# Kernel tuning notes

Hardware: AMD Instinct MI355X
Metric: run time of the kernel (lower is better)

## Reference

```python
import jax, jax.numpy as jnp
import numpy as np

B, N = 8192, 2048
_EPS = 1e-5


def setup_inputs() -> dict:
    key = jax.random.key(0)
    k1, k2, k3 = jax.random.split(key, 3)
    src = jax.random.normal(k1, (B, 3, N), dtype=jnp.float32)
    src_corr = jax.random.normal(k2, (B, 3, N), dtype=jnp.float32)
    weights = jax.random.uniform(k3, (B, N), dtype=jnp.float32)
    return {"src": src, "src_corr": src_corr, "weights": weights}


def reference(src, src_corr, weights):
    # src, src_corr: (B, 3, N); weights: (B, N)
    a = jnp.swapaxes(src, -1, -2)        # (B, N, 3)
    b = jnp.swapaxes(src_corr, -1, -2)   # (B, N, 3)
    w = weights[..., None]               # (B, N, 1)
    wn = w / (jnp.sum(w, axis=1, keepdims=True) + _EPS)
    centroid_a = jnp.sum(a * wn, axis=1)  # (B, 3)
    centroid_b = jnp.sum(b * wn, axis=1)  # (B, 3)
    a_c = a - centroid_a[:, None, :]
    b_c = b - centroid_b[:, None, :]
    # cov = a_c^T @ (b_c * wn) -> (B, 3, 3)
    cov = jnp.einsum('bnd,bne->bde', a_c, b_c * wn)
    u, s, vh = jnp.linalg.svd(cov, full_matrices=False)
    v = jnp.swapaxes(vh, -1, -2)
    ut = jnp.swapaxes(u, -1, -2)
    rot_pos = v @ ut
    v_neg = v.at[:, :, 2].multiply(-1.0)  # flip last column of v
    rot_neg = v_neg @ ut
    rot = jnp.where(jnp.linalg.det(rot_pos)[:, None, None] > 0, rot_pos, rot_neg)
    translation = centroid_b - jnp.einsum('bij,bj->bi', rot, centroid_a)  # (B, 3)
    return rot, translation
```

## Files before the change

kernel.cpp:

```cpp
#include <hip/hip_runtime.h>
#include <math.h>


constexpr int kB = 8192;
constexpr int kN = 2048;
constexpr float kEps = 1e-5f;
constexpr int kWavesPerBatch = 4;
constexpr int kIters = kN / 4 / 64 / kWavesPerBatch;

__global__ __launch_bounds__(256) void wproc_reduce(
    const float* __restrict__ src,
    const float* __restrict__ src_corr,
    const float* __restrict__ weights,
    float* __restrict__ ws)
{
    const int lane = threadIdx.x & 63;
    const int wave = threadIdx.x >> 6;
    const int b = blockIdx.x;

    const float* arow = src + (size_t)b * 3 * kN;
    const float* brow = src_corr + (size_t)b * 3 * kN;
    const float4* w4  = reinterpret_cast<const float4*>(weights + (size_t)b * kN);
    const float4* ax4 = reinterpret_cast<const float4*>(arow);
    const float4* ay4 = reinterpret_cast<const float4*>(arow + kN);
    const float4* az4 = reinterpret_cast<const float4*>(arow + 2 * kN);
    const float4* bx4 = reinterpret_cast<const float4*>(brow);
    const float4* by4 = reinterpret_cast<const float4*>(brow + kN);
    const float4* bz4 = reinterpret_cast<const float4*>(brow + 2 * kN);

    float acc[16];
#pragma unroll
    for (int i = 0; i < 16; ++i) acc[i] = 0.f;

#pragma unroll
    for (int it = 0; it < kIters; ++it) {
        const int idx = (wave * kIters + it) * 64 + lane;
        const float4 w  = w4[idx];
        const float4 ax = ax4[idx];
        const float4 ay = ay4[idx];
        const float4 az = az4[idx];
        const float4 bx = bx4[idx];
        const float4 by = by4[idx];
        const float4 bz = bz4[idx];
        const float wc[4]  = {w.x,  w.y,  w.z,  w.w};
        const float axc[4] = {ax.x, ax.y, ax.z, ax.w};
        const float ayc[4] = {ay.x, ay.y, ay.z, ay.w};
        const float azc[4] = {az.x, az.y, az.z, az.w};
        const float bxc[4] = {bx.x, bx.y, bx.z, bx.w};
        const float byc[4] = {by.x, by.y, by.z, by.w};
        const float bzc[4] = {bz.x, bz.y, bz.z, bz.w};
#pragma unroll
        for (int c = 0; c < 4; ++c) {
            const float ww  = wc[c];
            const float wax = ww * axc[c], way = ww * ayc[c], waz = ww * azc[c];
            const float bxx = bxc[c], byy = byc[c], bzz = bzc[c];
            acc[0]  += ww;
            acc[1]  += wax;                acc[2]  += way;                acc[3]  += waz;
            acc[4]  = fmaf(ww,  bxx, acc[4]);  acc[5]  = fmaf(ww,  byy, acc[5]);  acc[6]  = fmaf(ww,  bzz, acc[6]);
            acc[7]  = fmaf(wax, bxx, acc[7]);  acc[8]  = fmaf(wax, byy, acc[8]);  acc[9]  = fmaf(wax, bzz, acc[9]);
            acc[10] = fmaf(way, bxx, acc[10]); acc[11] = fmaf(way, byy, acc[11]); acc[12] = fmaf(way, bzz, acc[12]);
            acc[13] = fmaf(waz, bxx, acc[13]); acc[14] = fmaf(waz, byy, acc[14]); acc[15] = fmaf(waz, bzz, acc[15]);
        }
    }

#pragma unroll
    for (int i = 0; i < 16; ++i) {
        float v = acc[i];
#pragma unroll
        for (int off = 32; off > 0; off >>= 1)
            v += __shfl_down(v, off, 64);
        acc[i] = v;
    }

    __shared__ float part[kWavesPerBatch][16];
    if (lane == 0) {
#pragma unroll
        for (int i = 0; i < 16; ++i) part[wave][i] = acc[i];
    }
    __syncthreads();
    if (threadIdx.x < 16) {
        const int t = threadIdx.x;
        float s = part[0][t] + part[1][t] + part[2][t] + part[3][t];
        ws[(size_t)b * 16 + t] = s;
    }
}

__global__ __launch_bounds__(256) void wproc_solve(
    const float* __restrict__ ws,
    float* __restrict__ out)
{
    const int b = blockIdx.x * blockDim.x + threadIdx.x;
    if (b >= kB) return;

    float t[16];
#pragma unroll
    for (int i = 0; i < 4; ++i) {
        const float4 v = reinterpret_cast<const float4*>(ws + (size_t)b * 16)[i];
        t[4 * i] = v.x; t[4 * i + 1] = v.y; t[4 * i + 2] = v.z; t[4 * i + 3] = v.w;
    }

    const float W   = t[0];
    const float inv = 1.f / (W + kEps);
    const float S   = W * inv;
    float ca[3], cb[3];
#pragma unroll
    for (int d = 0; d < 3; ++d) { ca[d] = t[1 + d] * inv; cb[d] = t[4 + d] * inv; }

    float M[3][3];
    const float f2 = 2.f - S;
#pragma unroll
    for (int d = 0; d < 3; ++d)
#pragma unroll
        for (int e = 0; e < 3; ++e)
            M[d][e] = t[7 + 3 * d + e] * inv - ca[d] * cb[e] * f2;

    const float T  = M[0][0] + M[1][1] + M[2][2];
    const float cx = M[1][2] - M[2][1];
    const float cy = M[2][0] - M[0][2];
    const float cz = M[0][1] - M[1][0];
    float Nm[4][4];
    Nm[0][0] = T;
    Nm[0][1] = Nm[1][0] = cx;
    Nm[0][2] = Nm[2][0] = cy;
    Nm[0][3] = Nm[3][0] = cz;
    Nm[1][1] = 2.f * M[0][0] - T;
    Nm[2][2] = 2.f * M[1][1] - T;
    Nm[3][3] = 2.f * M[2][2] - T;
    Nm[1][2] = Nm[2][1] = M[0][1] + M[1][0];
    Nm[1][3] = Nm[3][1] = M[0][2] + M[2][0];
    Nm[2][3] = Nm[3][2] = M[1][2] + M[2][1];

    float Vv[4][4] = {{1,0,0,0},{0,1,0,0},{0,0,1,0},{0,0,0,1}};
    const int pp[6] = {0,0,0,1,1,2};
    const int qq[6] = {1,2,3,2,3,3};
    for (int sweep = 0; sweep < 6; ++sweep) {
        for (int r = 0; r < 6; ++r) {
            const int p = pp[r], q = qq[r];
            const float apq = Nm[p][q];
            if (fabsf(apq) < 1e-12f) continue;
            const float tau = (Nm[q][q] - Nm[p][p]) / (2.f * apq);
            const float tt  = copysignf(1.f, tau) / (fabsf(tau) + sqrtf(1.f + tau * tau));
            const float c   = 1.f / sqrtf(1.f + tt * tt);
            const float s   = tt * c;
            const float app = Nm[p][p], aqq = Nm[q][q];
            Nm[p][p] = app - tt * apq;
            Nm[q][q] = aqq + tt * apq;
            Nm[p][q] = Nm[q][p] = 0.f;
#pragma unroll
            for (int k = 0; k < 4; ++k) {
                if (k == p || k == q) continue;
                const float akp = Nm[k][p], akq = Nm[k][q];
                Nm[k][p] = Nm[p][k] = c * akp - s * akq;
                Nm[k][q] = Nm[q][k] = s * akp + c * akq;
            }
#pragma unroll
            for (int k = 0; k < 4; ++k) {
                const float vkp = Vv[k][p], vkq = Vv[k][q];
                Vv[k][p] = c * vkp - s * vkq;
                Vv[k][q] = s * vkp + c * vkq;
            }
        }
    }

    int jm = 0;
#pragma unroll
    for (int j = 1; j < 4; ++j) if (Nm[j][j] > Nm[jm][jm]) jm = j;
    float qw = Vv[0][jm], qx = Vv[1][jm], qy = Vv[2][jm], qz = Vv[3][jm];
    const float nq = 1.f / sqrtf(qw * qw + qx * qx + qy * qy + qz * qz);
    qw *= nq; qx *= nq; qy *= nq; qz *= nq;

    float R[3][3];
    R[0][0] = 1.f - 2.f * (qy * qy + qz * qz);
    R[0][1] = 2.f * (qx * qy - qw * qz);
    R[0][2] = 2.f * (qx * qz + qw * qy);
    R[1][0] = 2.f * (qx * qy + qw * qz);
    R[1][1] = 1.f - 2.f * (qx * qx + qz * qz);
    R[1][2] = 2.f * (qy * qz - qw * qx);
    R[2][0] = 2.f * (qx * qz - qw * qy);
    R[2][1] = 2.f * (qy * qz + qw * qx);
    R[2][2] = 1.f - 2.f * (qx * qx + qy * qy);

    float* ro = out + (size_t)b * 9;
#pragma unroll
    for (int i = 0; i < 3; ++i)
#pragma unroll
        for (int j = 0; j < 3; ++j)
            ro[3 * i + j] = R[i][j];

    float* to = out + (size_t)kB * 9 + (size_t)b * 3;
#pragma unroll
    for (int i = 0; i < 3; ++i)
        to[i] = cb[i] - (R[i][0] * ca[0] + R[i][1] * ca[1] + R[i][2] * ca[2]);
}

extern "C" void kernel_launch(void* const* d_in, const int* in_sizes, int n_in,
                              void* d_out, int out_size, void* d_ws, size_t ws_size,
                              hipStream_t stream) {
    const float* src      = (const float*)d_in[0];
    const float* src_corr = (const float*)d_in[1];
    const float* weights  = (const float*)d_in[2];
    float* out = (float*)d_out;
    float* ws  = (float*)d_ws;
    wproc_reduce<<<kB, 64 * kWavesPerBatch, 0, stream>>>(src, src_corr, weights, ws);
    wproc_solve<<<(kB + 255) / 256, 256, 0, stream>>>(ws, out);
}
```

Baseline: 443.2 us.

## Batch loads before compute, unroll Jacobi rotations statically, shrink solve blocks

In the reduce kernel, all global float4 loads are issued up front into register arrays before any accumulation, so more memory requests are in flight per wave. In the solve kernel, the Jacobi rotation pairs become template parameters, which removes dynamic register-array indexing and the scratch memory it can cause. Eigenvector selection uses register selects instead of an indexed lookup. The solve kernel is launched with 64-thread blocks to spread 8192 threads over more CUs, at the cost of higher register pressure in the reduce kernel.

```diff
diff --git a/kernel.cpp b/kernel.cpp
--- a/kernel.cpp
+++ b/kernel.cpp
@@ -28,27 +28,33 @@
     const float4* by4 = reinterpret_cast<const float4*>(brow + kN);
     const float4* bz4 = reinterpret_cast<const float4*>(brow + 2 * kN);
 
-    float acc[16];
-#pragma unroll
-    for (int i = 0; i < 16; ++i) acc[i] = 0.f;
-
+    float4 Lw[kIters], Lax[kIters], Lay[kIters], Laz[kIters];
+    float4 Lbx[kIters], Lby[kIters], Lbz[kIters];
 #pragma unroll
     for (int it = 0; it < kIters; ++it) {
         const int idx = (wave * kIters + it) * 64 + lane;
-        const float4 w  = w4[idx];
-        const float4 ax = ax4[idx];
-        const float4 ay = ay4[idx];
-        const float4 az = az4[idx];
-        const float4 bx = bx4[idx];
-        const float4 by = by4[idx];
-        const float4 bz = bz4[idx];
-        const float wc[4]  = {w.x,  w.y,  w.z,  w.w};
-        const float axc[4] = {ax.x, ax.y, ax.z, ax.w};
-        const float ayc[4] = {ay.x, ay.y, ay.z, ay.w};
-        const float azc[4] = {az.x, az.y, az.z, az.w};
-        const float bxc[4] = {bx.x, bx.y, bx.z, bx.w};
-        const float byc[4] = {by.x, by.y, by.z, by.w};
-        const float bzc[4] = {bz.x, bz.y, bz.z, bz.w};
+        Lw[it]  = w4[idx];
+        Lax[it] = ax4[idx];
+        Lay[it] = ay4[idx];
+        Laz[it] = az4[idx];
+        Lbx[it] = bx4[idx];
+        Lby[it] = by4[idx];
+        Lbz[it] = bz4[idx];
+    }
+
+    float acc[16];
+#pragma unroll
+    for (int i = 0; i < 16; ++i) acc[i] = 0.f;
+
+#pragma unroll
+    for (int it = 0; it < kIters; ++it) {
+        const float wc[4]  = {Lw[it].x,  Lw[it].y,  Lw[it].z,  Lw[it].w};
+        const float axc[4] = {Lax[it].x, Lax[it].y, Lax[it].z, Lax[it].w};
+        const float ayc[4] = {Lay[it].x, Lay[it].y, Lay[it].z, Lay[it].w};
+        const float azc[4] = {Laz[it].x, Laz[it].y, Laz[it].z, Laz[it].w};
+        const float bxc[4] = {Lbx[it].x, Lbx[it].y, Lbx[it].z, Lbx[it].w};
+        const float byc[4] = {Lby[it].x, Lby[it].y, Lby[it].z, Lby[it].w};
+        const float bzc[4] = {Lbz[it].x, Lbz[it].y, Lbz[it].z, Lbz[it].w};
 #pragma unroll
         for (int c = 0; c < 4; ++c) {
             const float ww  = wc[c];
@@ -85,7 +91,35 @@
     }
 }
 
-__global__ __launch_bounds__(256) void wproc_solve(
+template<int P, int Q>
+__device__ __forceinline__ void jrot(float (&Nm)[4][4], float (&Vv)[4][4]) {
+    const float apq = Nm[P][Q];
+    if (fabsf(apq) >= 1e-12f) {
+        const float tau = (Nm[Q][Q] - Nm[P][P]) / (2.f * apq);
+        const float tt  = copysignf(1.f, tau) / (fabsf(tau) + sqrtf(1.f + tau * tau));
+        const float c   = 1.f / sqrtf(1.f + tt * tt);
+        const float s   = tt * c;
+        const float app = Nm[P][P], aqq = Nm[Q][Q];
+        Nm[P][P] = app - tt * apq;
+        Nm[Q][Q] = aqq + tt * apq;
+        Nm[P][Q] = Nm[Q][P] = 0.f;
+#pragma unroll
+        for (int k = 0; k < 4; ++k) {
+            if (k == P || k == Q) continue;
+            const float akp = Nm[k][P], akq = Nm[k][Q];
+            Nm[k][P] = Nm[P][k] = c * akp - s * akq;
+            Nm[k][Q] = Nm[Q][k] = s * akp + c * akq;
+        }
+#pragma unroll
+        for (int k = 0; k < 4; ++k) {
+            const float vkp = Vv[k][P], vkq = Vv[k][Q];
+            Vv[k][P] = c * vkp - s * vkq;
+            Vv[k][Q] = s * vkp + c * vkq;
+        }
+    }
+}
+
+__global__ __launch_bounds__(64) void wproc_solve(
     const float* __restrict__ ws,
     float* __restrict__ out)
 {
@@ -131,41 +165,22 @@
     Nm[2][3] = Nm[3][2] = M[1][2] + M[2][1];
 
     float Vv[4][4] = {{1,0,0,0},{0,1,0,0},{0,0,1,0},{0,0,0,1}};
-    const int pp[6] = {0,0,0,1,1,2};
-    const int qq[6] = {1,2,3,2,3,3};
+
     for (int sweep = 0; sweep < 6; ++sweep) {
-        for (int r = 0; r < 6; ++r) {
-            const int p = pp[r], q = qq[r];
-            const float apq = Nm[p][q];
-            if (fabsf(apq) < 1e-12f) continue;
-            const float tau = (Nm[q][q] - Nm[p][p]) / (2.f * apq);
-            const float tt  = copysignf(1.f, tau) / (fabsf(tau) + sqrtf(1.f + tau * tau));
-            const float c   = 1.f / sqrtf(1.f + tt * tt);
-            const float s   = tt * c;
-            const float app = Nm[p][p], aqq = Nm[q][q];
-            Nm[p][p] = app - tt * apq;
-            Nm[q][q] = aqq + tt * apq;
-            Nm[p][q] = Nm[q][p] = 0.f;
-#pragma unroll
-            for (int k = 0; k < 4; ++k) {
-                if (k == p || k == q) continue;
-                const float akp = Nm[k][p], akq = Nm[k][q];
-                Nm[k][p] = Nm[p][k] = c * akp - s * akq;
-                Nm[k][q] = Nm[q][k] = s * akp + c * akq;
-            }
-#pragma unroll
-            for (int k = 0; k < 4; ++k) {
-                const float vkp = Vv[k][p], vkq = Vv[k][q];
-                Vv[k][p] = c * vkp - s * vkq;
-                Vv[k][q] = s * vkp + c * vkq;
-            }
-        }
-    }
-
-    int jm = 0;
-#pragma unroll
-    for (int j = 1; j < 4; ++j) if (Nm[j][j] > Nm[jm][jm]) jm = j;
-    float qw = Vv[0][jm], qx = Vv[1][jm], qy = Vv[2][jm], qz = Vv[3][jm];
+        jrot<0, 1>(Nm, Vv);
+        jrot<0, 2>(Nm, Vv);
+        jrot<0, 3>(Nm, Vv);
+        jrot<1, 2>(Nm, Vv);
+        jrot<1, 3>(Nm, Vv);
+        jrot<2, 3>(Nm, Vv);
+    }
+
+    float best = Nm[0][0];
+    float qw = Vv[0][0], qx = Vv[1][0], qy = Vv[2][0], qz = Vv[3][0];
+    if (Nm[1][1] > best) { best = Nm[1][1]; qw = Vv[0][1]; qx = Vv[1][1]; qy = Vv[2][1]; qz = Vv[3][1]; }
+    if (Nm[2][2] > best) { best = Nm[2][2]; qw = Vv[0][2]; qx = Vv[1][2]; qy = Vv[2][2]; qz = Vv[3][2]; }
+    if (Nm[3][3] > best) { best = Nm[3][3]; qw = Vv[0][3]; qx = Vv[1][3]; qy = Vv[2][3]; qz = Vv[3][3]; }
+
     const float nq = 1.f / sqrtf(qw * qw + qx * qx + qy * qy + qz * qz);
     qw *= nq; qx *= nq; qy *= nq; qz *= nq;
 
@@ -202,5 +217,5 @@
     float* out = (float*)d_out;
     float* ws  = (float*)d_ws;
     wproc_reduce<<<kB, 64 * kWavesPerBatch, 0, stream>>>(src, src_corr, weights, ws);
-    wproc_solve<<<(kB + 255) / 256, 256, 0, stream>>>(ws, out);
-}
+    wproc_solve<<<kB / 64, 64, 0, stream>>>(ws, out);
+}
```

Measured after the change: 434.0 us. -2.1%, faster.
